# Kernel optimization log

Measured on AMD Instinct MI355X. Metric: run time of the kernel, lower is better.

The kernel has to match this reference:

```python
import jax, jax.numpy as jnp
import numpy as np


def setup_inputs() -> dict:
    key = jax.random.key(0)
    ks = jax.random.split(key, 9)
    B, C, H, W = 1, 128, 96, 96
    Ci = C // 2
    s = 1.0 / np.sqrt(C)
    return {
        "x": jax.random.normal(ks[0], (B, C, H, W), dtype=jnp.float32),
        "theta_w": jax.random.normal(ks[1], (Ci, C), dtype=jnp.float32) * s,
        "theta_b": jax.random.normal(ks[2], (Ci,), dtype=jnp.float32) * 0.01,
        "phi_w": jax.random.normal(ks[3], (Ci, C), dtype=jnp.float32) * s,
        "phi_b": jax.random.normal(ks[4], (Ci,), dtype=jnp.float32) * 0.01,
        "g_w": jax.random.normal(ks[5], (Ci, C), dtype=jnp.float32) * s,
        "g_b": jax.random.normal(ks[6], (Ci,), dtype=jnp.float32) * 0.01,
        "out_w": jax.random.normal(ks[7], (C, Ci), dtype=jnp.float32) * (1.0 / np.sqrt(Ci)),
        "out_b": jax.random.normal(ks[8], (C,), dtype=jnp.float32) * 0.01,
    }


def reference(x, theta_w, theta_b, phi_w, phi_b, g_w, g_b, out_w, out_b):
    B, C, H, W = x.shape
    # 1x1 convs == per-position linear projections; flatten spatial to N tokens
    xf = x.transpose(0, 2, 3, 1).reshape(-1, C)          # (N, C), N = B*H*W
    theta = xf @ theta_w.T + theta_b                     # (N, Ci)
    phi = xf @ phi_w.T + phi_b                           # (N, Ci)
    g = xf @ g_w.T + g_b                                 # (N, Ci)
    # unscaled non-local attention with double softmax
    attn = jax.nn.softmax(theta @ phi.T, axis=-1)        # (N, N)
    y = jax.nn.softmax(attn @ g, axis=-1)                # (N, Ci)
    out = y @ out_w.T + out_b                            # (N, C)
    return out.reshape(B, H, W, C).transpose(0, 3, 1, 2) + x
```

## Files before the change

kernel.cpp:

```cpp
#include <hip/hip_runtime.h>
#include <hip/hip_bf16.h>

#define N_TOK 9216
#define C_IN  128
#define CI    64
#define SPLITS 8
#define L2E   1.44269504088896340736f

typedef __bf16 bf16x8 __attribute__((ext_vector_type(8)));
typedef unsigned short u16;
typedef u16 u16x4 __attribute__((ext_vector_type(4)));
typedef u16 u16x8 __attribute__((ext_vector_type(8)));
typedef unsigned u32x4 __attribute__((ext_vector_type(4)));
typedef float f32x4 __attribute__((ext_vector_type(4)));

static __device__ __forceinline__ u16 f2bf(float f) {
  return __builtin_bit_cast(u16, __float2bfloat16(f));
}
static __device__ __forceinline__ float bf2f(u16 b) {
  unsigned u = ((unsigned)b) << 16;
  return __builtin_bit_cast(float, u);
}
static __device__ __forceinline__ bf16x8 pack8(const float* f) {
  u16x8 t;
#pragma unroll
  for (int j = 0; j < 8; ++j) t[j] = f2bf(f[j]);
  return __builtin_bit_cast(bf16x8, t);
}
static __device__ __forceinline__ bf16x8 load_bf8(const u16* p) {
  u32x4 v = *(const u32x4*)p;
  return __builtin_bit_cast(bf16x8, v);
}
static __device__ __forceinline__ void gload_lds16(const void* g, void* l) {
  __builtin_amdgcn_global_load_lds(
      (const __attribute__((address_space(1))) void*)g,
      (__attribute__((address_space(3))) void*)l, 16, 0, 0);
}

#define MFMA16(a, b, c) __builtin_amdgcn_mfma_f32_16x16x32_bf16((a), (b), (c), 0, 0, 0)

__global__ __launch_bounds__(256) void k1_proj(
    const float* __restrict__ x,
    const float* __restrict__ tw, const float* __restrict__ tb,
    const float* __restrict__ pw, const float* __restrict__ pb,
    const float* __restrict__ gw, const float* __restrict__ gb,
    u16* __restrict__ thetaF, u16* __restrict__ phiF, u16* __restrict__ vF)
{
  __shared__ u16 sbuf[64 * 72];
  const int tid = threadIdx.x;
  const int w = tid >> 6, lane = tid & 63;
  const int lr = lane & 15, lg = lane >> 4;
  const int p0 = blockIdx.x * 64;

  bf16x8 bf[4][4];
#pragma unroll
  for (int nt = 0; nt < 4; ++nt) {
    const int p = p0 + nt * 16 + lr;
#pragma unroll
    for (int kc = 0; kc < 4; ++kc) {
      const int c0 = kc * 32 + lg * 8;
      float f[8];
#pragma unroll
      for (int j = 0; j < 8; ++j) f[j] = x[(c0 + j) * N_TOK + p];
      bf[nt][kc] = pack8(f);
    }
  }

  const float* Wm[3] = {tw, pw, gw};
  const float* Bm[3] = {tb, pb, gb};

#pragma unroll
  for (int m = 0; m < 3; ++m) {
    bf16x8 af[4];
#pragma unroll
    for (int kc = 0; kc < 4; ++kc) {
      const float* src = Wm[m] + (w * 16 + lr) * C_IN + kc * 32 + lg * 8;
      float f[8];
#pragma unroll
      for (int j = 0; j < 8; ++j) f[j] = src[j];
      af[kc] = pack8(f);
    }
    f32x4 acc[4];
#pragma unroll
    for (int nt = 0; nt < 4; ++nt) acc[nt] = f32x4{0.f, 0.f, 0.f, 0.f};
#pragma unroll
    for (int kc = 0; kc < 4; ++kc)
#pragma unroll
      for (int nt = 0; nt < 4; ++nt)
        acc[nt] = MFMA16(af[kc], bf[nt][kc], acc[nt]);

    float bias[4];
#pragma unroll
    for (int r = 0; r < 4; ++r) bias[r] = Bm[m][w * 16 + lg * 4 + r];

    const float oscale = (m == 0) ? L2E : 1.0f;

    if (m < 2) {
#pragma unroll
      for (int nt = 0; nt < 4; ++nt)
#pragma unroll
        for (int r = 0; r < 4; ++r)
          sbuf[(nt * 16 + lr) * 72 + (w * 16 + lg * 4 + r)] =
              f2bf((acc[nt][r] + bias[r]) * oscale);
      __syncthreads();
      if (m == 0) {
#pragma unroll
        for (int e = 0; e < 2; ++e) {
          const int ch = tid * 2 + e;
          const int ln = ch & 63, c = (ch >> 6) & 1, qt = ch >> 7;
          const int ql = qt * 16 + (ln & 15), d = c * 32 + (ln >> 4) * 8;
          u32x4 v = *(const u32x4*)&sbuf[ql * 72 + d];
          *(u32x4*)&thetaF[(((size_t)(p0 / 16 + qt) * 2 + c) * 64 + ln) * 8] = v;
        }
      } else {
#pragma unroll
        for (int e = 0; e < 2; ++e) {
          const int ch = tid * 2 + e;
          const int ln = ch & 63, i = (ch >> 6) & 3, t = ch >> 8;
          const int kl = t * 32 + (i >> 1) * 16 + (ln & 15);
          const int d = (i & 1) * 32 + (ln >> 4) * 8;
          u32x4 v = *(const u32x4*)&sbuf[kl * 72 + d];
          *(u32x4*)&phiF[(((size_t)(p0 / 32 + t) * 4 + i) * 64 + ln) * 8] = v;
        }
      }
      __syncthreads();
    } else {
#pragma unroll
      for (int nt = 0; nt < 4; ++nt)
#pragma unroll
        for (int r = 0; r < 4; ++r)
          sbuf[(w * 16 + lg * 4 + r) * 72 + nt * 16 + lr] = f2bf(acc[nt][r] + bias[r]);
      __syncthreads();
#pragma unroll
      for (int e = 0; e < 2; ++e) {
        const int ch = tid * 2 + e;
        const int ln = ch & 63, n = (ch >> 6) & 3, t = ch >> 8;
        const int d = n * 16 + (ln & 15), g4 = (ln >> 4) * 4;
        u16x4 lo = *(const u16x4*)&sbuf[d * 72 + t * 32 + g4];
        u16x4 hi = *(const u16x4*)&sbuf[d * 72 + t * 32 + 16 + g4];
        u16x8 v;
#pragma unroll
        for (int j = 0; j < 4; ++j) { v[j] = lo[j]; v[4 + j] = hi[j]; }
        *(u16x8*)&vF[(((size_t)(p0 / 32 + t) * 4 + n) * 64 + ln) * 8] = v;
      }
    }
  }
}

__global__ __launch_bounds__(256) void k2_flash(
    const u16* __restrict__ thetaF, const u16* __restrict__ phiF,
    const u16* __restrict__ vF,
    u16* __restrict__ Opart, float* __restrict__ Lpart)
{
  __shared__ u16 kvbuf[2][16][512];
  const int tid = threadIdx.x;
  const int w = tid >> 6, lane = tid & 63;
  const int lr = lane & 15, g = lane >> 4;
  const int ks = blockIdx.x & 7;
  const int qt = blockIdx.x >> 3;
  const int q0 = qt * 64 + w * 16;
  const int NT64 = (N_TOK / SPLITS) / 64;
  const int t64base = ks * NT64;

  const bf16x8 qb0 = load_bf8(&thetaF[(((size_t)(q0 / 16) * 2 + 0) * 64 + lane) * 8]);
  const bf16x8 qb1 = load_bf8(&thetaF[(((size_t)(q0 / 16) * 2 + 1) * 64 + lane) * 8]);

  f32x4 o[4], o4;
#pragma unroll
  for (int n = 0; n < 4; ++n) o[n] = f32x4{0.f, 0.f, 0.f, 0.f};
  o4 = f32x4{0.f, 0.f, 0.f, 0.f};

  u16x8 onesw;
#pragma unroll
  for (int j = 0; j < 8; ++j) onesw[j] = 0x3F80;
  const bf16x8 ones = __builtin_bit_cast(bf16x8, onesw);

  const u16* sbase = (w < 2) ? phiF : vF;
  const int sub = w & 1;
  const int fbase = w * 4;

#define STAGE(T, buf)                                                          \
  {                                                                            \
    const u16* gp = sbase + ((size_t)(2 * (t64base + (T)) + sub) * 4) * 512 +  \
                    lane * 8;                                                  \
    gload_lds16(gp,        &kvbuf[buf][fbase][0]);                             \
    gload_lds16(gp + 512,  &kvbuf[buf][fbase + 1][0]);                         \
    gload_lds16(gp + 1024, &kvbuf[buf][fbase + 2][0]);                         \
    gload_lds16(gp + 1536, &kvbuf[buf][fbase + 3][0]);                         \
  }

  STAGE(0, 0);
  __syncthreads();

  int cur = 0;
  for (int T = 0; T < NT64; ++T) {
    if (T + 1 < NT64) STAGE(T + 1, cur ^ 1);

#pragma unroll
    for (int h = 0; h < 2; ++h) {
      const bf16x8 ka0 = load_bf8(&kvbuf[cur][h * 4 + 0][lane * 8]);
      const bf16x8 ka1 = load_bf8(&kvbuf[cur][h * 4 + 1][lane * 8]);
      const bf16x8 ka2 = load_bf8(&kvbuf[cur][h * 4 + 2][lane * 8]);
      const bf16x8 ka3 = load_bf8(&kvbuf[cur][h * 4 + 3][lane * 8]);
      bf16x8 va[4];
#pragma unroll
      for (int n = 0; n < 4; ++n) va[n] = load_bf8(&kvbuf[cur][8 + h * 4 + n][lane * 8]);

      f32x4 s0 = f32x4{0.f, 0.f, 0.f, 0.f}, s1 = f32x4{0.f, 0.f, 0.f, 0.f};
      s0 = MFMA16(ka0, qb0, s0); s0 = MFMA16(ka1, qb1, s0);
      s1 = MFMA16(ka2, qb0, s1); s1 = MFMA16(ka3, qb1, s1);

      float p0v[4], p1v[4];
#pragma unroll
      for (int r = 0; r < 4; ++r) {
        p0v[r] = __builtin_amdgcn_exp2f(s0[r]);
        p1v[r] = __builtin_amdgcn_exp2f(s1[r]);
      }
      u16x8 pw;
#pragma unroll
      for (int r = 0; r < 4; ++r) { pw[r] = f2bf(p0v[r]); pw[4 + r] = f2bf(p1v[r]); }
      const bf16x8 pb = __builtin_bit_cast(bf16x8, pw);
#pragma unroll
      for (int n = 0; n < 4; ++n) o[n] = MFMA16(va[n], pb, o[n]);
      o4 = MFMA16(ones, pb, o4);
    }

    __syncthreads();
    cur ^= 1;
  }

  const int qg = ks * N_TOK + q0;
#pragma unroll
  for (int n = 0; n < 4; ++n) {
    u16x4 ov;
#pragma unroll
    for (int r = 0; r < 4; ++r) ov[r] = f2bf(o[n][r]);
    *(u16x4*)&Opart[(size_t)(qg + lr) * CI + n * 16 + 4 * g] = ov;
  }
  if (lane < 16) Lpart[qg + lr] = o4[0];
}

__global__ __launch_bounds__(256) void k2b_combine(
    const u16* __restrict__ Opart, const float* __restrict__ Lpart,
    u16* __restrict__ y)
{
  const int tid = threadIdx.x;
  const int w = tid >> 6, lane = tid & 63;
  const int q = blockIdx.x * 4 + w;

  float L = 0.f, acc = 0.f;
#pragma unroll
  for (int k = 0; k < SPLITS; ++k) {
    L += Lpart[k * N_TOK + q];
    acc += bf2f(Opart[(size_t)(k * N_TOK + q) * CI + lane]);
  }
  const float ypre = acc / L;

  float mx = ypre;
#pragma unroll
  for (int off = 1; off <= 32; off <<= 1) mx = fmaxf(mx, __shfl_xor(mx, off, 64));
  const float e = __builtin_amdgcn_exp2f((ypre - mx) * L2E);
  float s = e;
#pragma unroll
  for (int off = 1; off <= 32; off <<= 1) s += __shfl_xor(s, off, 64);
  y[q * CI + lane] = f2bf(e / s);
}

__global__ __launch_bounds__(256) void k3_out(
    const u16* __restrict__ y, const float* __restrict__ ow,
    const float* __restrict__ ob, const float* __restrict__ x,
    float* __restrict__ out)
{
  const int tid = threadIdx.x;
  const int w = tid >> 6, lane = tid & 63;
  const int lr = lane & 15, lg = lane >> 4;
  const int p0 = blockIdx.x * 32;

  bf16x8 yb[2][2];
#pragma unroll
  for (int nt = 0; nt < 2; ++nt)
#pragma unroll
    for (int kc = 0; kc < 2; ++kc)
      yb[nt][kc] = load_bf8(&y[(p0 + nt * 16 + lr) * CI + kc * 32 + lg * 8]);

#pragma unroll
  for (int mt = 0; mt < 2; ++mt) {
    bf16x8 af[2];
#pragma unroll
    for (int kc = 0; kc < 2; ++kc) {
      const float* src = ow + (w * 32 + mt * 16 + lr) * CI + kc * 32 + lg * 8;
      float f[8];
#pragma unroll
      for (int j = 0; j < 8; ++j) f[j] = src[j];
      af[kc] = pack8(f);
    }
#pragma unroll
    for (int nt = 0; nt < 2; ++nt) {
      f32x4 acc = f32x4{0.f, 0.f, 0.f, 0.f};
      acc = MFMA16(af[0], yb[nt][0], acc);
      acc = MFMA16(af[1], yb[nt][1], acc);
#pragma unroll
      for (int r = 0; r < 4; ++r) {
        const int c = w * 32 + mt * 16 + lg * 4 + r;
        const int p = p0 + nt * 16 + lr;
        out[(size_t)c * N_TOK + p] = acc[r] + ob[c] + x[(size_t)c * N_TOK + p];
      }
    }
  }
}

extern "C" void kernel_launch(void* const* d_in, const int* in_sizes, int n_in,
                              void* d_out, int out_size, void* d_ws, size_t ws_size,
                              hipStream_t stream) {
  const float* x  = (const float*)d_in[0];
  const float* tw = (const float*)d_in[1];
  const float* tb = (const float*)d_in[2];
  const float* pw = (const float*)d_in[3];
  const float* pb = (const float*)d_in[4];
  const float* gw = (const float*)d_in[5];
  const float* gb = (const float*)d_in[6];
  const float* ow = (const float*)d_in[7];
  const float* ob = (const float*)d_in[8];
  float* out = (float*)d_out;

  char* ws = (char*)d_ws;
  u16* thetaF = (u16*)(ws);
  u16* phiF   = (u16*)(ws + 1179648);
  u16* vF     = (u16*)(ws + 2 * 1179648);
  u16* yb     = (u16*)(ws + 3 * 1179648);
  u16* Op     = (u16*)(ws + 4 * 1179648);
  float* Lp   = (float*)(ws + 4 * 1179648 + 9437184);

  hipLaunchKernelGGL(k1_proj, dim3(144), dim3(256), 0, stream,
                     x, tw, tb, pw, pb, gw, gb, thetaF, phiF, vF);
  hipLaunchKernelGGL(k2_flash, dim3(144 * SPLITS), dim3(256), 0, stream,
                     thetaF, phiF, vF, Op, Lp);
  hipLaunchKernelGGL(k2b_combine, dim3(N_TOK / 4), dim3(256), 0, stream,
                     Op, Lp, yb);
  hipLaunchKernelGGL(k3_out, dim3(288), dim3(256), 0, stream,
                     yb, ow, ob, x, out);
}
```

Before: 60.81 us.

## Split projection kernel across grid.y and load V fragments directly from global

The projection kernel now launches one block per (token tile, projection) pair via grid.y instead of looping over three projections in one block. This triples the grid size for better occupancy, at the cost of reloading the x tile three times. In the flash kernel, V fragments are read straight from global memory into registers each tile rather than staged through LDS. This halves the LDS buffer and the async copies, but exposes global load latency inside the loop and raises register pressure.

```diff
diff --git a/kernel.cpp b/kernel.cpp
--- a/kernel.cpp
+++ b/kernel.cpp
@@ -51,6 +51,7 @@
   const int w = tid >> 6, lane = tid & 63;
   const int lr = lane & 15, lg = lane >> 4;
   const int p0 = blockIdx.x * 64;
+  const int m = blockIdx.y;
 
   bf16x8 bf[4][4];
 #pragma unroll
@@ -66,83 +67,79 @@
     }
   }
 
-  const float* Wm[3] = {tw, pw, gw};
-  const float* Bm[3] = {tb, pb, gb};
-
-#pragma unroll
-  for (int m = 0; m < 3; ++m) {
-    bf16x8 af[4];
-#pragma unroll
-    for (int kc = 0; kc < 4; ++kc) {
-      const float* src = Wm[m] + (w * 16 + lr) * C_IN + kc * 32 + lg * 8;
-      float f[8];
-#pragma unroll
-      for (int j = 0; j < 8; ++j) f[j] = src[j];
-      af[kc] = pack8(f);
-    }
-    f32x4 acc[4];
-#pragma unroll
-    for (int nt = 0; nt < 4; ++nt) acc[nt] = f32x4{0.f, 0.f, 0.f, 0.f};
-#pragma unroll
-    for (int kc = 0; kc < 4; ++kc)
-#pragma unroll
-      for (int nt = 0; nt < 4; ++nt)
-        acc[nt] = MFMA16(af[kc], bf[nt][kc], acc[nt]);
-
-    float bias[4];
-#pragma unroll
-    for (int r = 0; r < 4; ++r) bias[r] = Bm[m][w * 16 + lg * 4 + r];
-
-    const float oscale = (m == 0) ? L2E : 1.0f;
-
-    if (m < 2) {
-#pragma unroll
-      for (int nt = 0; nt < 4; ++nt)
-#pragma unroll
-        for (int r = 0; r < 4; ++r)
-          sbuf[(nt * 16 + lr) * 72 + (w * 16 + lg * 4 + r)] =
-              f2bf((acc[nt][r] + bias[r]) * oscale);
-      __syncthreads();
-      if (m == 0) {
-#pragma unroll
-        for (int e = 0; e < 2; ++e) {
-          const int ch = tid * 2 + e;
-          const int ln = ch & 63, c = (ch >> 6) & 1, qt = ch >> 7;
-          const int ql = qt * 16 + (ln & 15), d = c * 32 + (ln >> 4) * 8;
-          u32x4 v = *(const u32x4*)&sbuf[ql * 72 + d];
-          *(u32x4*)&thetaF[(((size_t)(p0 / 16 + qt) * 2 + c) * 64 + ln) * 8] = v;
-        }
-      } else {
-#pragma unroll
-        for (int e = 0; e < 2; ++e) {
-          const int ch = tid * 2 + e;
-          const int ln = ch & 63, i = (ch >> 6) & 3, t = ch >> 8;
-          const int kl = t * 32 + (i >> 1) * 16 + (ln & 15);
-          const int d = (i & 1) * 32 + (ln >> 4) * 8;
-          u32x4 v = *(const u32x4*)&sbuf[kl * 72 + d];
-          *(u32x4*)&phiF[(((size_t)(p0 / 32 + t) * 4 + i) * 64 + ln) * 8] = v;
-        }
-      }
-      __syncthreads();
-    } else {
-#pragma unroll
-      for (int nt = 0; nt < 4; ++nt)
-#pragma unroll
-        for (int r = 0; r < 4; ++r)
-          sbuf[(w * 16 + lg * 4 + r) * 72 + nt * 16 + lr] = f2bf(acc[nt][r] + bias[r]);
-      __syncthreads();
+  const float* Wm = (m == 0) ? tw : (m == 1) ? pw : gw;
+  const float* Bm = (m == 0) ? tb : (m == 1) ? pb : gb;
+
+  bf16x8 af[4];
+#pragma unroll
+  for (int kc = 0; kc < 4; ++kc) {
+    const float* src = Wm + (w * 16 + lr) * C_IN + kc * 32 + lg * 8;
+    float f[8];
+#pragma unroll
+    for (int j = 0; j < 8; ++j) f[j] = src[j];
+    af[kc] = pack8(f);
+  }
+  f32x4 acc[4];
+#pragma unroll
+  for (int nt = 0; nt < 4; ++nt) acc[nt] = f32x4{0.f, 0.f, 0.f, 0.f};
+#pragma unroll
+  for (int kc = 0; kc < 4; ++kc)
+#pragma unroll
+    for (int nt = 0; nt < 4; ++nt)
+      acc[nt] = MFMA16(af[kc], bf[nt][kc], acc[nt]);
+
+  float bias[4];
+#pragma unroll
+  for (int r = 0; r < 4; ++r) bias[r] = Bm[w * 16 + lg * 4 + r];
+
+  const float oscale = (m == 0) ? L2E : 1.0f;
+
+  if (m < 2) {
+#pragma unroll
+    for (int nt = 0; nt < 4; ++nt)
+#pragma unroll
+      for (int r = 0; r < 4; ++r)
+        sbuf[(nt * 16 + lr) * 72 + (w * 16 + lg * 4 + r)] =
+            f2bf((acc[nt][r] + bias[r]) * oscale);
+    __syncthreads();
+    if (m == 0) {
 #pragma unroll
       for (int e = 0; e < 2; ++e) {
         const int ch = tid * 2 + e;
-        const int ln = ch & 63, n = (ch >> 6) & 3, t = ch >> 8;
-        const int d = n * 16 + (ln & 15), g4 = (ln >> 4) * 4;
-        u16x4 lo = *(const u16x4*)&sbuf[d * 72 + t * 32 + g4];
-        u16x4 hi = *(const u16x4*)&sbuf[d * 72 + t * 32 + 16 + g4];
-        u16x8 v;
-#pragma unroll
-        for (int j = 0; j < 4; ++j) { v[j] = lo[j]; v[4 + j] = hi[j]; }
-        *(u16x8*)&vF[(((size_t)(p0 / 32 + t) * 4 + n) * 64 + ln) * 8] = v;
+        const int ln = ch & 63, c = (ch >> 6) & 1, qt = ch >> 7;
+        const int ql = qt * 16 + (ln & 15), d = c * 32 + (ln >> 4) * 8;
+        u32x4 v = *(const u32x4*)&sbuf[ql * 72 + d];
+        *(u32x4*)&thetaF[(((size_t)(p0 / 16 + qt) * 2 + c) * 64 + ln) * 8] = v;
       }
+    } else {
+#pragma unroll
+      for (int e = 0; e < 2; ++e) {
+        const int ch = tid * 2 + e;
+        const int ln = ch & 63, i = (ch >> 6) & 3, t = ch >> 8;
+        const int kl = t * 32 + (i >> 1) * 16 + (ln & 15);
+        const int d = (i & 1) * 32 + (ln >> 4) * 8;
+        u32x4 v = *(const u32x4*)&sbuf[kl * 72 + d];
+        *(u32x4*)&phiF[(((size_t)(p0 / 32 + t) * 4 + i) * 64 + ln) * 8] = v;
+      }
+    }
+  } else {
+#pragma unroll
+    for (int nt = 0; nt < 4; ++nt)
+#pragma unroll
+      for (int r = 0; r < 4; ++r)
+        sbuf[(w * 16 + lg * 4 + r) * 72 + nt * 16 + lr] = f2bf(acc[nt][r] + bias[r]);
+    __syncthreads();
+#pragma unroll
+    for (int e = 0; e < 2; ++e) {
+      const int ch = tid * 2 + e;
+      const int ln = ch & 63, n = (ch >> 6) & 3, t = ch >> 8;
+      const int d = n * 16 + (ln & 15), g4 = (ln >> 4) * 4;
+      u16x4 lo = *(const u16x4*)&sbuf[d * 72 + t * 32 + g4];
+      u16x4 hi = *(const u16x4*)&sbuf[d * 72 + t * 32 + 16 + g4];
+      u16x8 v;
+#pragma unroll
+      for (int j = 0; j < 4; ++j) { v[j] = lo[j]; v[4 + j] = hi[j]; }
+      *(u16x8*)&vF[(((size_t)(p0 / 32 + t) * 4 + n) * 64 + ln) * 8] = v;
     }
   }
 }
@@ -152,7 +149,7 @@
     const u16* __restrict__ vF,
     u16* __restrict__ Opart, float* __restrict__ Lpart)
 {
-  __shared__ u16 kvbuf[2][16][512];
+  __shared__ u16 kvbuf[2][8][512];
   const int tid = threadIdx.x;
   const int w = tid >> 6, lane = tid & 63;
   const int lr = lane & 15, g = lane >> 4;
@@ -175,18 +172,15 @@
   for (int j = 0; j < 8; ++j) onesw[j] = 0x3F80;
   const bf16x8 ones = __builtin_bit_cast(bf16x8, onesw);
 
-  const u16* sbase = (w < 2) ? phiF : vF;
-  const int sub = w & 1;
-  const int fbase = w * 4;
-
-#define STAGE(T, buf)                                                          \
-  {                                                                            \
-    const u16* gp = sbase + ((size_t)(2 * (t64base + (T)) + sub) * 4) * 512 +  \
-                    lane * 8;                                                  \
-    gload_lds16(gp,        &kvbuf[buf][fbase][0]);                             \
-    gload_lds16(gp + 512,  &kvbuf[buf][fbase + 1][0]);                         \
-    gload_lds16(gp + 1024, &kvbuf[buf][fbase + 2][0]);                         \
-    gload_lds16(gp + 1536, &kvbuf[buf][fbase + 3][0]);                         \
+  const int f0 = 2 * w;
+  const size_t kgoff = (size_t)(f0 & 3) * 512 + lane * 8;
+  const int hW = w >> 1;
+
+#define STAGE(T, buf)                                                         \
+  {                                                                           \
+    const u16* gp = phiF + (size_t)(2 * (t64base + (T)) + hW) * 2048 + kgoff; \
+    gload_lds16(gp, &kvbuf[buf][f0][0]);                                      \
+    gload_lds16(gp + 512, &kvbuf[buf][f0 + 1][0]);                            \
   }
 
   STAGE(0, 0);
@@ -194,6 +188,14 @@
 
   int cur = 0;
   for (int T = 0; T < NT64; ++T) {
+    bf16x8 va[2][4];
+    const u16* pV = vF + (size_t)(2 * (t64base + T)) * 2048 + lane * 8;
+#pragma unroll
+    for (int h = 0; h < 2; ++h)
+#pragma unroll
+      for (int n = 0; n < 4; ++n)
+        va[h][n] = load_bf8(pV + (size_t)(h * 4 + n) * 512);
+
     if (T + 1 < NT64) STAGE(T + 1, cur ^ 1);
 
 #pragma unroll
@@ -202,9 +204,6 @@
       const bf16x8 ka1 = load_bf8(&kvbuf[cur][h * 4 + 1][lane * 8]);
       const bf16x8 ka2 = load_bf8(&kvbuf[cur][h * 4 + 2][lane * 8]);
       const bf16x8 ka3 = load_bf8(&kvbuf[cur][h * 4 + 3][lane * 8]);
-      bf16x8 va[4];
-#pragma unroll
-      for (int n = 0; n < 4; ++n) va[n] = load_bf8(&kvbuf[cur][8 + h * 4 + n][lane * 8]);
 
       f32x4 s0 = f32x4{0.f, 0.f, 0.f, 0.f}, s1 = f32x4{0.f, 0.f, 0.f, 0.f};
       s0 = MFMA16(ka0, qb0, s0); s0 = MFMA16(ka1, qb1, s0);
@@ -221,7 +220,7 @@
       for (int r = 0; r < 4; ++r) { pw[r] = f2bf(p0v[r]); pw[4 + r] = f2bf(p1v[r]); }
       const bf16x8 pb = __builtin_bit_cast(bf16x8, pw);
 #pragma unroll
-      for (int n = 0; n < 4; ++n) o[n] = MFMA16(va[n], pb, o[n]);
+      for (int n = 0; n < 4; ++n) o[n] = MFMA16(va[h][n], pb, o[n]);
       o4 = MFMA16(ones, pb, o4);
     }
 
@@ -331,7 +330,7 @@
   u16* Op     = (u16*)(ws + 4 * 1179648);
   float* Lp   = (float*)(ws + 4 * 1179648 + 9437184);
 
-  hipLaunchKernelGGL(k1_proj, dim3(144), dim3(256), 0, stream,
+  hipLaunchKernelGGL(k1_proj, dim3(144, 3), dim3(256), 0, stream,
                      x, tw, tb, pw, pb, gw, gb, thetaF, phiF, vF);
   hipLaunchKernelGGL(k2_flash, dim3(144 * SPLITS), dim3(256), 0, stream,
                      thetaF, phiF, vF, Op, Lp);
```

New measurement: 59.19 us. 1.03x faster.
